# Performance work log

Measured on AMD Instinct MI355X. Metric: run time of the kernel, lower is better.

## Reference

```python
import jax, jax.numpy as jnp
import numpy as np

NUM_ITEMS = 50000
EMBED = 256
HEADS = 8
HEAD_DIM = EMBED // HEADS
B, S = 32, 512
NEG_BIG = -1e9   # mask fill for dot-product scores
NEG_SMALL = -1e5 # mask fill for rel / time maps (as in RKT)


def setup_inputs() -> dict:
    key = jax.random.key(0)
    ks = jax.random.split(key, 20)
    sc = 0.02
    return {
        "item_inputs": jax.random.randint(ks[0], (B, S), 0, NUM_ITEMS + 1),
        "label_inputs": jax.random.randint(ks[1], (B, S), 0, 2, dtype=jnp.int32),
        "item_ids": jax.random.randint(ks[2], (B, S), 0, NUM_ITEMS + 1),
        "rel": jax.random.uniform(ks[3], (B, S, S), jnp.float32),
        "timestamp": jax.random.uniform(ks[4], (B, S, S), jnp.float32) * 10.0,
        # learned params
        "item_embeds": jax.random.normal(ks[5], (NUM_ITEMS + 1, EMBED), jnp.float32) * sc,
        "W_in": jax.random.normal(ks[6], (2 * EMBED, EMBED), jnp.float32) * sc,
        "b_in": jnp.zeros((EMBED,), jnp.float32),
        "Wq": jax.random.normal(ks[7], (EMBED, EMBED), jnp.float32) * sc,
        "bq": jnp.zeros((EMBED,), jnp.float32),
        "Wk": jax.random.normal(ks[8], (EMBED, EMBED), jnp.float32) * sc,
        "bk": jnp.zeros((EMBED,), jnp.float32),
        "Wv": jax.random.normal(ks[9], (EMBED, EMBED), jnp.float32) * sc,
        "bv": jnp.zeros((EMBED,), jnp.float32),
        "W_out": jax.random.normal(ks[10], (EMBED, 1), jnp.float32) * sc,
        "b_out": jnp.zeros((1,), jnp.float32),
        "l1": jnp.float32(0.5),
        "l2": jnp.float32(0.5),
    }


def _split_heads(t, W, b):
    # [B,S,E] -> [B,H,S,HD]
    return (t @ W + b).reshape(B, S, HEADS, HEAD_DIM).transpose(0, 2, 1, 3)


def reference(item_inputs, label_inputs, item_ids, rel, timestamp, item_embeds,
              W_in, b_in, Wq, bq, Wk, bk, Wv, bv, W_out, b_out, l1, l2):
    # --- input construction: response-gated duplicated item embedding ---
    e = item_embeds[item_inputs]                       # [B,S,E]
    lab = label_inputs[..., None].astype(e.dtype)      # [B,S,1]
    inputs = jnp.concatenate([e * lab, e * (1.0 - lab)], axis=-1)  # [B,S,2E]
    inputs = jax.nn.relu(inputs @ W_in + b_in)         # [B,S,E]
    query = item_embeds[item_ids]                      # [B,S,E]

    future = jnp.triu(jnp.ones((S, S), bool), 1)       # True above diagonal

    Q = _split_heads(query, Wq, bq)
    K = _split_heads(inputs, Wk, bk)
    V = _split_heads(inputs, Wv, bv)

    # scaled dot-product scores with causal mask
    scores = jnp.einsum('bhqd,bhkd->bhqk', Q, K) / np.float32(np.sqrt(HEAD_DIM))
    prob_attn = jax.nn.softmax(jnp.where(future, NEG_BIG, scores), axis=-1)

    # relational (item-item correlation) attention, future-masked
    rel_m = rel * (~future).astype(rel.dtype)          # [B,S,S]
    rel_attn = jax.nn.softmax(jnp.where(rel_m == 0, NEG_SMALL, rel_m), axis=-1)
    rel_attn = rel_attn[:, None]                       # broadcast over heads

    # exponential time-decay attention, future-masked
    ts = jnp.exp(-jnp.abs(timestamp))
    time_attn = jax.nn.softmax(jnp.where(future, NEG_SMALL, ts), axis=-1)[:, None]

    attn = (1.0 - l2) * prob_attn + l2 * time_attn
    attn = (1.0 - l1) * attn + l1 * rel_attn           # [B,H,S,S]

    out = jnp.einsum('bhqk,bhkd->bhqd', attn, V)       # [B,H,S,HD]
    out = out.transpose(0, 2, 1, 3).reshape(B, S, EMBED)
    logits = out @ W_out + b_out                       # [B,S,1]
    return logits, attn
```

## Files before the change

kernel.cpp:

```cpp
#include <hip/hip_runtime.h>
#include <hip/hip_bf16.h>

#define SEQ 512
#define EMB 256
#define NHEAD 8
#define HD 32

using bf16x8 = __attribute__((ext_vector_type(8))) short;
using f32x4  = __attribute__((ext_vector_type(4))) float;

static __device__ __forceinline__ unsigned short f2bf(float x) {
    union { float f; unsigned int u; } v; v.f = x;
    unsigned int r = v.u + 0x7FFFu + ((v.u >> 16) & 1u);
    return (unsigned short)(r >> 16);
}
static __device__ __forceinline__ float bf2f(unsigned short v) {
    union { unsigned int u; float f; } w; w.u = ((unsigned int)v) << 16; return w.f;
}

__global__ __launch_bounds__(256) void fused_prep_kernel(
    const int* __restrict__ item_inputs,
    const int* __restrict__ label_inputs,
    const int* __restrict__ item_ids,
    const float* __restrict__ embeds,
    const float* __restrict__ W_in,
    const float* __restrict__ Wq,
    const float* __restrict__ Wk,
    const float* __restrict__ Wv,
    const float* __restrict__ Wout,
    const float* __restrict__ bv,
    const float* __restrict__ bout,
    const float* __restrict__ rel,
    const float* __restrict__ tsp,
    unsigned short* __restrict__ Abig,
    unsigned short* __restrict__ qbf,
    unsigned short* __restrict__ WTin,
    unsigned short* __restrict__ WTq,
    unsigned short* __restrict__ WTk,
    float* __restrict__ Wvw,
    float* __restrict__ bvw,
    float* __restrict__ logits,
    float* __restrict__ dent,
    float* __restrict__ denr)
{
    const int bid = blockIdx.x;
    const int t = threadIdx.x;

    if (bid < 1024) {
        const int b = bid >> 5;
        const int s16 = 31 - (bid & 31);
        const int q0 = s16 * 16;
        const int row = t >> 4;
        const int lane16 = t & 15;
        const int qrow = q0 + row;
        const size_t base = ((size_t)(b * SEQ) + qrow) * SEQ;
        float dt = 0.f, dr = 0.f;
        for (int k4 = lane16 * 4; k4 <= qrow; k4 += 64) {
            float4 tv4 = *(const float4*)(tsp + base + k4);
            float4 rv4 = *(const float4*)(rel + base + k4);
            const float* tvp = &tv4.x;
            const float* rvp = &rv4.x;
            #pragma unroll
            for (int j = 0; j < 4; j++) {
                const bool va = (k4 + j) <= qrow;
                dt += va ? __expf(__expf(-fabsf(tvp[j]))) : 0.f;
                dr += (va && rvp[j] != 0.f) ? __expf(rvp[j]) : 0.f;
            }
        }
        dt += __shfl_xor(dt, 1); dt += __shfl_xor(dt, 2);
        dt += __shfl_xor(dt, 4); dt += __shfl_xor(dt, 8);
        dr += __shfl_xor(dr, 1); dr += __shfl_xor(dr, 2);
        dr += __shfl_xor(dr, 4); dr += __shfl_xor(dr, 8);
        if (lane16 == 0) {
            dent[b * SEQ + qrow] = dt;
            denr[b * SEQ + qrow] = dr;
        }
    } else if (bid < 5120) {
        int r = (bid - 1024) * 4 + (t >> 6);
        int j = (t & 63) * 4;
        int item = item_inputs[r];
        int lab  = label_inputs[r];
        int qid  = item_ids[r];
        float4 e4 = *(const float4*)(embeds + (size_t)item * EMB + j);
        ushort4 on  = make_ushort4(f2bf(e4.x), f2bf(e4.y), f2bf(e4.z), f2bf(e4.w));
        ushort4 off = make_ushort4(0, 0, 0, 0);
        *(ushort4*)(Abig + (size_t)r * 512 + j)       = lab ? on : off;
        *(ushort4*)(Abig + (size_t)r * 512 + 256 + j) = lab ? off : on;
        float4 q4 = *(const float4*)(embeds + (size_t)qid * EMB + j);
        *(ushort4*)(qbf + (size_t)r * 256 + j) =
            make_ushort4(f2bf(q4.x), f2bf(q4.y), f2bf(q4.z), f2bf(q4.w));
    } else {
        int idx = (bid - 5120) * 256 + t;
        if (idx < 131072) {
            int n = idx >> 9, k = idx & 511;
            WTin[idx] = f2bf(W_in[(size_t)k * 256 + n]);
        } else if (idx < 196608) {
            int i = idx - 131072;
            int n = i >> 8, k = i & 255;
            WTq[i] = f2bf(Wq[(size_t)k * 256 + n]);
        } else if (idx < 262144) {
            int i = idx - 196608;
            int n = i >> 8, k = i & 255;
            WTk[i] = f2bf(Wk[(size_t)k * 256 + n]);
        } else if (idx < 264192) {
            int i = idx - 262144;
            int c = i >> 3, h = i & 7;
            float s = 0.f;
            #pragma unroll
            for (int d = 0; d < 32; d++)
                s += Wv[(size_t)c * 256 + h * 32 + d] * Wout[h * 32 + d];
            Wvw[i] = s;
        } else if (idx < 264200) {
            int h = idx - 264192;
            float s = 0.f;
            #pragma unroll
            for (int d = 0; d < 32; d++) s += bv[h * 32 + d] * Wout[h * 32 + d];
            bvw[h] = s;
        } else if (idx < 280584) {
            logits[idx - 264200] = bout[0];
        }
    }
}

template<int KDIM, int RELU, int OUTBF>
static __device__ __forceinline__ void gemm_body(
    const unsigned short* __restrict__ A,
    const unsigned short* __restrict__ BT,
    const float* __restrict__ bias,
    void* __restrict__ Cout, float scale)
{
    __shared__ unsigned short As[64][40];
    __shared__ unsigned short Bs[128][40];
    const int t = threadIdx.x;
    const int row0 = blockIdx.x * 64;
    const int col0 = blockIdx.y * 128;
    const int wid = t >> 6, lane = t & 63;
    const int wm = wid & 1, wn = wid >> 1;
    const int lg = lane >> 4, l15 = lane & 15;

    f32x4 acc[2][4];
    #pragma unroll
    for (int i = 0; i < 2; i++)
        #pragma unroll
        for (int j = 0; j < 4; j++) acc[i][j] = (f32x4){0.f, 0.f, 0.f, 0.f};

    const int arow = t >> 2, achk = t & 3;
    const int brow = t >> 1, bhalf = t & 1;

    for (int k0 = 0; k0 < KDIM; k0 += 32) {
        __syncthreads();
        *(uint4*)(&As[arow][achk * 8]) =
            *(const uint4*)(A + (size_t)(row0 + arow) * KDIM + k0 + achk * 8);
        const unsigned short* bsrc = BT + (size_t)(col0 + brow) * KDIM + k0 + bhalf * 16;
        *(uint4*)(&Bs[brow][bhalf * 16])     = *(const uint4*)(bsrc);
        *(uint4*)(&Bs[brow][bhalf * 16 + 8]) = *(const uint4*)(bsrc + 8);
        __syncthreads();
        bf16x8 af[2], bfr[4];
        #pragma unroll
        for (int fm = 0; fm < 2; fm++)
            af[fm] = *(const bf16x8*)(&As[wm * 32 + fm * 16 + l15][lg * 8]);
        #pragma unroll
        for (int fn = 0; fn < 4; fn++)
            bfr[fn] = *(const bf16x8*)(&Bs[wn * 64 + fn * 16 + l15][lg * 8]);
        #pragma unroll
        for (int fm = 0; fm < 2; fm++)
            #pragma unroll
            for (int fn = 0; fn < 4; fn++)
                acc[fm][fn] = __builtin_amdgcn_mfma_f32_16x16x32_bf16(
                    af[fm], bfr[fn], acc[fm][fn], 0, 0, 0);
    }
    #pragma unroll
    for (int fm = 0; fm < 2; fm++)
        #pragma unroll
        for (int fn = 0; fn < 4; fn++) {
            int col = col0 + wn * 64 + fn * 16 + l15;
            float bvv = bias[col];
            #pragma unroll
            for (int r = 0; r < 4; r++) {
                int row = row0 + wm * 32 + fm * 16 + lg * 4 + r;
                float v = acc[fm][fn][r] + bvv;
                if (RELU) v = fmaxf(v, 0.f);
                v *= scale;
                if (OUTBF) ((unsigned short*)Cout)[(size_t)row * 256 + col] = f2bf(v);
                else       ((float*)Cout)[(size_t)row * 256 + col] = v;
            }
        }
}

__global__ __launch_bounds__(256, 2) void gemmA_kernel(
    const unsigned short* __restrict__ Abig,
    const unsigned short* __restrict__ WTin,
    const float* __restrict__ b_in,
    unsigned short* __restrict__ Xbf,
    const unsigned short* __restrict__ qbf,
    const unsigned short* __restrict__ WTq,
    const float* __restrict__ bq,
    unsigned short* __restrict__ Qbf)
{
    if (blockIdx.z == 0)
        gemm_body<512, 1, 1>(Abig, WTin, b_in, (void*)Xbf, 1.0f);
    else
        gemm_body<256, 0, 1>(qbf, WTq, bq, (void*)Qbf, 0.17677669529663687f);
}

static __device__ __forceinline__ void vw_body(
    const unsigned short* __restrict__ Xbf,
    const float* __restrict__ Wvw,
    const float* __restrict__ bvw,
    float* __restrict__ Vw)
{
    __shared__ float sW[2048];
    __shared__ float sb[8];
    int t = threadIdx.x;
    #pragma unroll
    for (int i = 0; i < 8; i++) sW[i * 256 + t] = Wvw[i * 256 + t];
    if (t < 8) sb[t] = bvw[t];
    __syncthreads();
    int row = blockIdx.x * 256 + t;
    float acc[8];
    #pragma unroll
    for (int h = 0; h < 8; h++) acc[h] = sb[h];
    for (int d0 = 0; d0 < 32; d0++) {
        bf16x8 x = *(const bf16x8*)(Xbf + (size_t)row * 256 + d0 * 8);
        #pragma unroll
        for (int j = 0; j < 8; j++) {
            float xf = bf2f((unsigned short)x[j]);
            #pragma unroll
            for (int h = 0; h < 8; h++) acc[h] += xf * sW[(d0 * 8 + j) * 8 + h];
        }
    }
    *(float4*)(Vw + (size_t)row * 8)     = make_float4(acc[0], acc[1], acc[2], acc[3]);
    *(float4*)(Vw + (size_t)row * 8 + 4) = make_float4(acc[4], acc[5], acc[6], acc[7]);
}

__global__ __launch_bounds__(256, 2) void gemmB_kernel(
    const unsigned short* __restrict__ Xbf,
    const unsigned short* __restrict__ WTk,
    const float* __restrict__ bk,
    unsigned short* __restrict__ Kbf,
    const float* __restrict__ Wvw,
    const float* __restrict__ bvw,
    float* __restrict__ Vw)
{
    if (blockIdx.z == 0) {
        gemm_body<256, 0, 1>(Xbf, WTk, bk, (void*)Kbf, 1.0f);
    } else {
        if (blockIdx.x >= 64 || blockIdx.y != 0) return;
        vw_body(Xbf, Wvw, bvw, Vw);
    }
}

__global__ __launch_bounds__(256, 8) void attnW_kernel(
    const unsigned short* __restrict__ Qbf,
    const unsigned short* __restrict__ Kbf,
    const float* __restrict__ Vw,
    const float* __restrict__ rel,
    const float* __restrict__ tsp,
    const float* __restrict__ dent,
    const float* __restrict__ denr,
    const float* __restrict__ pl1,
    const float* __restrict__ pl2,
    float* __restrict__ logits,
    float* __restrict__ attn)
{
    __shared__ unsigned short sP[16][520];
    __shared__ float sVw[512];
    __shared__ float sden[4][16];

    const int t = threadIdx.x;
    const int id = blockIdx.x;
    const int qt16 = 31 - (id >> 8);
    const int b = (id >> 3) & 31;
    const int h = id & 7;
    const int q0 = qt16 * 16;
    const int qmax = q0 + 15;

    const int w = t >> 6, lane = t & 63;
    const int l15 = lane & 15, lg = lane >> 4;

    const float l1 = pl1[0], l2 = pl2[0];
    const float cp = (1.f - l1) * (1.f - l2);
    const float ct = (1.f - l1) * l2;
    const float cr = l1;

    sVw[t]       = Vw[((size_t)(b * SEQ) + t) * 8 + h];
    sVw[256 + t] = Vw[((size_t)(b * SEQ) + 256 + t) * 8 + h];

    bf16x8 aq = *(const bf16x8*)(Qbf + (size_t)(b * SEQ + q0 + l15) * EMB + h * 32 + lg * 8);

    float dp[4] = {0.f, 0.f, 0.f, 0.f};
    #pragma unroll
    for (int ki = 0; ki < 4; ki++) {
        const int kt = w + ki * 4;
        const int k0 = kt * 32;
        if (k0 <= qmax) {
            #pragma unroll
            for (int nf = 0; nf < 2; nf++) {
                const int kcol = k0 + nf * 16 + l15;
                bf16x8 bk = *(const bf16x8*)(Kbf +
                    (size_t)(b * SEQ + kcol) * EMB + h * 32 + lg * 8);
                f32x4 am = __builtin_amdgcn_mfma_f32_16x16x32_bf16(
                    aq, bk, (f32x4){0.f, 0.f, 0.f, 0.f}, 0, 0, 0);
                #pragma unroll
                for (int r = 0; r < 4; r++) {
                    const int qloc = lg * 4 + r;
                    float e = (kcol <= q0 + qloc) ? __expf(am[r]) : 0.f;
                    sP[qloc][kcol] = f2bf(e);
                    dp[r] += e;
                }
            }
        } else {
            #pragma unroll
            for (int nf = 0; nf < 2; nf++)
                #pragma unroll
                for (int r = 0; r < 4; r++)
                    sP[lg * 4 + r][k0 + nf * 16 + l15] = 0;
        }
    }
    #pragma unroll
    for (int r = 0; r < 4; r++) {
        float v = dp[r];
        v += __shfl_xor(v, 1); v += __shfl_xor(v, 2);
        v += __shfl_xor(v, 4); v += __shfl_xor(v, 8);
        if (l15 == 0) sden[w][lg * 4 + r] = v;
    }
    __syncthreads();

    const int wrow = t >> 4;
    const int wcol = (t & 15) * 4;
    const int qrow_w = q0 + wrow;
    const float den = sden[0][wrow] + sden[1][wrow] + sden[2][wrow] + sden[3][wrow];
    const float cpinv = cp / den;
    const float dtv = dent[b * SEQ + qrow_w];
    const float drv = denr[b * SEQ + qrow_w];
    const float ctt = ct / dtv;
    const float crr = drv > 0.f ? cr / drv : 0.f;

    float* arow = attn + ((size_t)((b * NHEAD + h) * SEQ) + qrow_w) * SEQ;
    const size_t rbase = ((size_t)(b * SEQ) + qrow_w) * SEQ;
    const f32x4 z4 = (f32x4){0.f, 0.f, 0.f, 0.f};
    float plog = 0.f;

    #pragma unroll
    for (int s = 0; s < 8; s++) {
        const int c = wcol + s * 64;
        f32x4 o;
        if (c > qrow_w) {
            o = z4;
        } else {
            float4 tv4 = *(const float4*)(tsp + rbase + c);
            float4 rv4 = *(const float4*)(rel + rbase + c);
            ushort4 p4 = *(const ushort4*)(&sP[wrow][c]);
            const float* tvp = &tv4.x;
            const float* rvp = &rv4.x;
            const unsigned short* pp = &p4.x;
            #pragma unroll
            for (int j = 0; j < 4; j++) {
                const bool va = (c + j) <= qrow_w;
                float e_t = va ? __expf(__expf(-fabsf(tvp[j]))) * ctt : 0.f;
                float e_r = (va && rvp[j] != 0.f) ? __expf(rvp[j]) * crr : 0.f;
                float a = fmaf(bf2f(pp[j]), cpinv, e_t + e_r);
                a = va ? a : 0.f;
                o[j] = a;
                plog = fmaf(a, sVw[c + j], plog);
            }
        }
        __builtin_nontemporal_store(o, (f32x4*)(arow + c));
    }

    plog += __shfl_xor(plog, 1); plog += __shfl_xor(plog, 2);
    plog += __shfl_xor(plog, 4); plog += __shfl_xor(plog, 8);
    if ((t & 15) == 0)
        atomicAdd(&logits[b * SEQ + qrow_w], plog);
}

extern "C" void kernel_launch(void* const* d_in, const int* in_sizes, int n_in,
                              void* d_out, int out_size, void* d_ws, size_t ws_size,
                              hipStream_t stream)
{
    (void)in_sizes; (void)n_in; (void)out_size; (void)ws_size;
    const int*   item_inputs  = (const int*)d_in[0];
    const int*   label_inputs = (const int*)d_in[1];
    const int*   item_ids     = (const int*)d_in[2];
    const float* rel   = (const float*)d_in[3];
    const float* tsp   = (const float*)d_in[4];
    const float* emb   = (const float*)d_in[5];
    const float* W_in  = (const float*)d_in[6];
    const float* b_in  = (const float*)d_in[7];
    const float* Wq    = (const float*)d_in[8];
    const float* bq    = (const float*)d_in[9];
    const float* Wk    = (const float*)d_in[10];
    const float* bk    = (const float*)d_in[11];
    const float* Wv    = (const float*)d_in[12];
    const float* bv    = (const float*)d_in[13];
    const float* Wout  = (const float*)d_in[14];
    const float* bout  = (const float*)d_in[15];
    const float* l1    = (const float*)d_in[16];
    const float* l2    = (const float*)d_in[17];

    const size_t R = 16384;
    char* w = (char*)d_ws;
    unsigned short* Abig = (unsigned short*)w; w += R * 512 * 2;
    unsigned short* qbf  = (unsigned short*)w; w += R * 256 * 2;
    unsigned short* WTin = (unsigned short*)w; w += (size_t)256 * 512 * 2;
    unsigned short* WTq  = (unsigned short*)w; w += (size_t)256 * 256 * 2;
    unsigned short* WTk  = (unsigned short*)w; w += (size_t)256 * 256 * 2;
    unsigned short* Xbf  = (unsigned short*)w; w += R * 256 * 2;
    unsigned short* Qbf  = (unsigned short*)w; w += R * 256 * 2;
    unsigned short* Kbf  = (unsigned short*)w; w += R * 256 * 2;
    float* Wvw  = (float*)w; w += 2048 * 4;
    float* Vw   = (float*)w; w += R * 8 * 4;
    float* bvw  = (float*)w; w += 256;
    float* dent = (float*)w; w += (size_t)32 * SEQ * 4;
    float* denr = (float*)w; w += (size_t)32 * SEQ * 4;

    float* logits = (float*)d_out;
    float* attnp  = (float*)d_out + 16384;

    fused_prep_kernel<<<dim3(6217), dim3(256), 0, stream>>>(
        item_inputs, label_inputs, item_ids, emb,
        W_in, Wq, Wk, Wv, Wout, bv, bout, rel, tsp,
        Abig, qbf, WTin, WTq, WTk, Wvw, bvw, logits, dent, denr);

    gemmA_kernel<<<dim3(256, 2, 2), dim3(256), 0, stream>>>(
        Abig, WTin, b_in, Xbf, qbf, WTq, bq, Qbf);

    gemmB_kernel<<<dim3(256, 2, 2), dim3(256), 0, stream>>>(
        Xbf, WTk, bk, Kbf, Wvw, bvw, Vw);

    attnW_kernel<<<dim3(8192), dim3(256), 0, stream>>>(
        Qbf, Kbf, Vw, rel, tsp, dent, denr, l1, l2, logits, attnp);
}
```

Baseline: 145.2 us.

## Offload zero-fill of upper-triangular attention tiles into earlier kernels

The strictly-future 64x64 tiles of the attention output are now zero-filled with nontemporal stores by extra blocks added to the prep and the two GEMM kernels. The attention kernel then loops only up to the diagonal tile for each row and skips zeroing the softmax scratch beyond it. The goal is to take the zero-write bandwidth off the critical attention kernel and overlap it with compute-light stages. This adds cross-kernel coupling through tile-index bookkeeping, and the grids must stay exactly in step with that bookkeeping.

After: 227.1 us. +56.4%, slower.

```diff
diff --git a/kernel.cpp b/kernel.cpp
--- a/kernel.cpp
+++ b/kernel.cpp
@@ -16,6 +16,34 @@
 }
 static __device__ __forceinline__ float bf2f(unsigned short v) {
     union { unsigned int u; float f; } w; w.u = ((unsigned int)v) << 16; return w.f;
+}
+
+static __device__ __forceinline__ void zfill_work(int idx, int t,
+                                                  float* __restrict__ attn)
+{
+    const f32x4 z4 = (f32x4){0.f, 0.f, 0.f, 0.f};
+    #pragma unroll
+    for (int i = 0; i < 4; i++) {
+        int ti = idx * 4 + i;
+        int bh = ti / 28;
+        int tt = ti - bh * 28;
+        int s = 0, pre = 0;
+        #pragma unroll
+        for (int ss = 0; ss < 6; ss++) {
+            int cnt = 7 - s;
+            bool adv = tt >= pre + cnt;
+            pre += adv ? cnt : 0;
+            s   += adv ? 1 : 0;
+        }
+        int j = tt - pre;
+        int row = 64 * s + (t >> 2);
+        int col = 64 * (s + 1) + 64 * j + (t & 3) * 16;
+        float* p = attn + ((size_t)bh * SEQ + row) * SEQ + col;
+        __builtin_nontemporal_store(z4, (f32x4*)(p));
+        __builtin_nontemporal_store(z4, (f32x4*)(p + 4));
+        __builtin_nontemporal_store(z4, (f32x4*)(p + 8));
+        __builtin_nontemporal_store(z4, (f32x4*)(p + 12));
+    }
 }
 
 __global__ __launch_bounds__(256) void fused_prep_kernel(
@@ -41,7 +69,8 @@
     float* __restrict__ bvw,
     float* __restrict__ logits,
     float* __restrict__ dent,
-    float* __restrict__ denr)
+    float* __restrict__ denr,
+    float* __restrict__ attn)
 {
     const int bid = blockIdx.x;
     const int t = threadIdx.x;
@@ -89,7 +118,7 @@
         float4 q4 = *(const float4*)(embeds + (size_t)qid * EMB + j);
         *(ushort4*)(qbf + (size_t)r * 256 + j) =
             make_ushort4(f2bf(q4.x), f2bf(q4.y), f2bf(q4.z), f2bf(q4.w));
-    } else {
+    } else if (bid < 6217) {
         int idx = (bid - 5120) * 256 + t;
         if (idx < 131072) {
             int n = idx >> 9, k = idx & 511;
@@ -119,6 +148,8 @@
         } else if (idx < 280584) {
             logits[idx - 264200] = bout[0];
         }
+    } else {
+        zfill_work(bid - 6217, t, attn);
     }
 }
 
@@ -195,12 +226,15 @@
     const unsigned short* __restrict__ qbf,
     const unsigned short* __restrict__ WTq,
     const float* __restrict__ bq,
-    unsigned short* __restrict__ Qbf)
+    unsigned short* __restrict__ Qbf,
+    float* __restrict__ attn)
 {
     if (blockIdx.z == 0)
         gemm_body<512, 1, 1>(Abig, WTin, b_in, (void*)Xbf, 1.0f);
+    else if (blockIdx.z == 1)
+        gemm_body<256, 0, 1>(qbf, WTq, bq, (void*)Qbf, 0.17677669529663687f);
     else
-        gemm_body<256, 0, 1>(qbf, WTq, bq, (void*)Qbf, 0.17677669529663687f);
+        zfill_work(768 + (blockIdx.y << 8) + blockIdx.x, threadIdx.x, attn);
 }
 
 static __device__ __forceinline__ void vw_body(
@@ -240,13 +274,16 @@
     unsigned short* __restrict__ Kbf,
     const float* __restrict__ Wvw,
     const float* __restrict__ bvw,
-    float* __restrict__ Vw)
+    float* __restrict__ Vw,
+    float* __restrict__ attn)
 {
     if (blockIdx.z == 0) {
         gemm_body<256, 0, 1>(Xbf, WTk, bk, (void*)Kbf, 1.0f);
-    } else {
+    } else if (blockIdx.z == 1) {
         if (blockIdx.x >= 64 || blockIdx.y != 0) return;
         vw_body(Xbf, Wvw, bvw, Vw);
+    } else {
+        zfill_work(1280 + (blockIdx.y << 8) + blockIdx.x, threadIdx.x, attn);
     }
 }
 
@@ -309,7 +346,7 @@
                     dp[r] += e;
                 }
             }
-        } else {
+        } else if (k0 <= qmax + 64) {
             #pragma unroll
             for (int nf = 0; nf < 2; nf++)
                 #pragma unroll
@@ -329,6 +366,7 @@
     const int wrow = t >> 4;
     const int wcol = (t & 15) * 4;
     const int qrow_w = q0 + wrow;
+    const int smax = qrow_w >> 6;
     const float den = sden[0][wrow] + sden[1][wrow] + sden[2][wrow] + sden[3][wrow];
     const float cpinv = cp / den;
     const float dtv = dent[b * SEQ + qrow_w];
@@ -341,8 +379,7 @@
     const f32x4 z4 = (f32x4){0.f, 0.f, 0.f, 0.f};
     float plog = 0.f;
 
-    #pragma unroll
-    for (int s = 0; s < 8; s++) {
+    for (int s = 0; s <= smax; s++) {
         const int c = wcol + s * 64;
         f32x4 o;
         if (c > qrow_w) {
@@ -417,16 +454,16 @@
     float* logits = (float*)d_out;
     float* attnp  = (float*)d_out + 16384;
 
-    fused_prep_kernel<<<dim3(6217), dim3(256), 0, stream>>>(
+    fused_prep_kernel<<<dim3(6985), dim3(256), 0, stream>>>(
         item_inputs, label_inputs, item_ids, emb,
         W_in, Wq, Wk, Wv, Wout, bv, bout, rel, tsp,
-        Abig, qbf, WTin, WTq, WTk, Wvw, bvw, logits, dent, denr);
-
-    gemmA_kernel<<<dim3(256, 2, 2), dim3(256), 0, stream>>>(
-        Abig, WTin, b_in, Xbf, qbf, WTq, bq, Qbf);
-
-    gemmB_kernel<<<dim3(256, 2, 2), dim3(256), 0, stream>>>(
-        Xbf, WTk, bk, Kbf, Wvw, bvw, Vw);
+        Abig, qbf, WTin, WTq, WTk, Wvw, bvw, logits, dent, denr, attnp);
+
+    gemmA_kernel<<<dim3(256, 2, 3), dim3(256), 0, stream>>>(
+        Abig, WTin, b_in, Xbf, qbf, WTq, bq, Qbf, attnp);
+
+    gemmB_kernel<<<dim3(256, 2, 3), dim3(256), 0, stream>>>(
+        Xbf, WTk, bk, Kbf, Wvw, bvw, Vw, attnp);
 
     attnW_kernel<<<dim3(8192), dim3(256), 0, stream>>>(
         Qbf, Kbf, Vw, rel, tsp, dent, denr, l1, l2, logits, attnp);
```

## Fuse head loop into attention kernel and cache rel/time numerators in LDS

Applied to the files above, without the earlier changes.

The time/rel softmax denominator pass moves out of the prep kernel and into the attention kernel. Each block now handles one (batch, 16-query tile) and loops over all 8 heads, so the rel and timestamp rows are read from global memory once instead of once per head. Their exponentials are stored as packed bf16 in shared memory, and Vw is written head-major so it can be loaded directly. Logits are written directly instead of accumulated atomically. The trade-offs are fewer blocks (1024) with larger LDS use and lower occupancy, a serial head loop with two barriers per head, and bf16 rounding of the rel/time numerators.

Result: slower. 150.2 us (+3.4%).

```diff
diff --git a/kernel.cpp b/kernel.cpp
--- a/kernel.cpp
+++ b/kernel.cpp
@@ -30,8 +30,6 @@
     const float* __restrict__ Wout,
     const float* __restrict__ bv,
     const float* __restrict__ bout,
-    const float* __restrict__ rel,
-    const float* __restrict__ tsp,
     unsigned short* __restrict__ Abig,
     unsigned short* __restrict__ qbf,
     unsigned short* __restrict__ WTin,
@@ -39,44 +37,13 @@
     unsigned short* __restrict__ WTk,
     float* __restrict__ Wvw,
     float* __restrict__ bvw,
-    float* __restrict__ logits,
-    float* __restrict__ dent,
-    float* __restrict__ denr)
+    float* __restrict__ logits)
 {
     const int bid = blockIdx.x;
     const int t = threadIdx.x;
 
-    if (bid < 1024) {
-        const int b = bid >> 5;
-        const int s16 = 31 - (bid & 31);
-        const int q0 = s16 * 16;
-        const int row = t >> 4;
-        const int lane16 = t & 15;
-        const int qrow = q0 + row;
-        const size_t base = ((size_t)(b * SEQ) + qrow) * SEQ;
-        float dt = 0.f, dr = 0.f;
-        for (int k4 = lane16 * 4; k4 <= qrow; k4 += 64) {
-            float4 tv4 = *(const float4*)(tsp + base + k4);
-            float4 rv4 = *(const float4*)(rel + base + k4);
-            const float* tvp = &tv4.x;
-            const float* rvp = &rv4.x;
-            #pragma unroll
-            for (int j = 0; j < 4; j++) {
-                const bool va = (k4 + j) <= qrow;
-                dt += va ? __expf(__expf(-fabsf(tvp[j]))) : 0.f;
-                dr += (va && rvp[j] != 0.f) ? __expf(rvp[j]) : 0.f;
-            }
-        }
-        dt += __shfl_xor(dt, 1); dt += __shfl_xor(dt, 2);
-        dt += __shfl_xor(dt, 4); dt += __shfl_xor(dt, 8);
-        dr += __shfl_xor(dr, 1); dr += __shfl_xor(dr, 2);
-        dr += __shfl_xor(dr, 4); dr += __shfl_xor(dr, 8);
-        if (lane16 == 0) {
-            dent[b * SEQ + qrow] = dt;
-            denr[b * SEQ + qrow] = dr;
-        }
-    } else if (bid < 5120) {
-        int r = (bid - 1024) * 4 + (t >> 6);
+    if (bid < 4096) {
+        int r = bid * 4 + (t >> 6);
         int j = (t & 63) * 4;
         int item = item_inputs[r];
         int lab  = label_inputs[r];
@@ -90,7 +57,7 @@
         *(ushort4*)(qbf + (size_t)r * 256 + j) =
             make_ushort4(f2bf(q4.x), f2bf(q4.y), f2bf(q4.z), f2bf(q4.w));
     } else {
-        int idx = (bid - 5120) * 256 + t;
+        int idx = (bid - 4096) * 256 + t;
         if (idx < 131072) {
             int n = idx >> 9, k = idx & 511;
             WTin[idx] = f2bf(W_in[(size_t)k * 256 + n]);
@@ -207,7 +174,7 @@
     const unsigned short* __restrict__ Xbf,
     const float* __restrict__ Wvw,
     const float* __restrict__ bvw,
-    float* __restrict__ Vw)
+    float* __restrict__ VwT)
 {
     __shared__ float sW[2048];
     __shared__ float sb[8];
@@ -229,8 +196,10 @@
             for (int h = 0; h < 8; h++) acc[h] += xf * sW[(d0 * 8 + j) * 8 + h];
         }
     }
-    *(float4*)(Vw + (size_t)row * 8)     = make_float4(acc[0], acc[1], acc[2], acc[3]);
-    *(float4*)(Vw + (size_t)row * 8 + 4) = make_float4(acc[4], acc[5], acc[6], acc[7]);
+    const int bb = row >> 9, rr = row & 511;
+    #pragma unroll
+    for (int h = 0; h < 8; h++)
+        VwT[((size_t)(bb * NHEAD + h)) * SEQ + rr] = acc[h];
 }
 
 __global__ __launch_bounds__(256, 2) void gemmB_kernel(
@@ -240,38 +209,37 @@
     unsigned short* __restrict__ Kbf,
     const float* __restrict__ Wvw,
     const float* __restrict__ bvw,
-    float* __restrict__ Vw)
+    float* __restrict__ VwT)
 {
     if (blockIdx.z == 0) {
         gemm_body<256, 0, 1>(Xbf, WTk, bk, (void*)Kbf, 1.0f);
     } else {
         if (blockIdx.x >= 64 || blockIdx.y != 0) return;
-        vw_body(Xbf, Wvw, bvw, Vw);
-    }
-}
-
-__global__ __launch_bounds__(256, 8) void attnW_kernel(
+        vw_body(Xbf, Wvw, bvw, VwT);
+    }
+}
+
+__global__ __launch_bounds__(256, 3) void attnF_kernel(
     const unsigned short* __restrict__ Qbf,
     const unsigned short* __restrict__ Kbf,
-    const float* __restrict__ Vw,
+    const float* __restrict__ VwT,
     const float* __restrict__ rel,
     const float* __restrict__ tsp,
-    const float* __restrict__ dent,
-    const float* __restrict__ denr,
+    const float* __restrict__ bout,
     const float* __restrict__ pl1,
     const float* __restrict__ pl2,
     float* __restrict__ logits,
     float* __restrict__ attn)
 {
+    __shared__ unsigned int   sNum[16][520];
     __shared__ unsigned short sP[16][520];
-    __shared__ float sVw[512];
     __shared__ float sden[4][16];
+    __shared__ float sctt[16], scrr[16];
 
     const int t = threadIdx.x;
     const int id = blockIdx.x;
-    const int qt16 = 31 - (id >> 8);
-    const int b = (id >> 3) & 31;
-    const int h = id & 7;
+    const int b = id >> 5;
+    const int qt16 = 31 - (id & 31);
     const int q0 = qt16 * 16;
     const int qmax = q0 + 15;
 
@@ -283,95 +251,115 @@
     const float ct = (1.f - l1) * l2;
     const float cr = l1;
 
-    sVw[t]       = Vw[((size_t)(b * SEQ) + t) * 8 + h];
-    sVw[256 + t] = Vw[((size_t)(b * SEQ) + 256 + t) * 8 + h];
-
-    bf16x8 aq = *(const bf16x8*)(Qbf + (size_t)(b * SEQ + q0 + l15) * EMB + h * 32 + lg * 8);
-
-    float dp[4] = {0.f, 0.f, 0.f, 0.f};
-    #pragma unroll
-    for (int ki = 0; ki < 4; ki++) {
-        const int kt = w + ki * 4;
-        const int k0 = kt * 32;
-        if (k0 <= qmax) {
-            #pragma unroll
-            for (int nf = 0; nf < 2; nf++) {
-                const int kcol = k0 + nf * 16 + l15;
-                bf16x8 bk = *(const bf16x8*)(Kbf +
-                    (size_t)(b * SEQ + kcol) * EMB + h * 32 + lg * 8);
-                f32x4 am = __builtin_amdgcn_mfma_f32_16x16x32_bf16(
-                    aq, bk, (f32x4){0.f, 0.f, 0.f, 0.f}, 0, 0, 0);
+    const int wrow = t >> 4;
+    const int lane16 = t & 15;
+    const int qrow_w = q0 + wrow;
+    const size_t rbase = ((size_t)(b * SEQ) + qrow_w) * SEQ;
+
+    float dt = 0.f, dr = 0.f;
+    for (int k4 = lane16 * 4; k4 <= qrow_w; k4 += 64) {
+        float4 tv4 = *(const float4*)(tsp + rbase + k4);
+        float4 rv4 = *(const float4*)(rel + rbase + k4);
+        const float* tvp = &tv4.x;
+        const float* rvp = &rv4.x;
+        unsigned int pk[4];
+        #pragma unroll
+        for (int j = 0; j < 4; j++) {
+            const bool va = (k4 + j) <= qrow_w;
+            float et = va ? __expf(__expf(-fabsf(tvp[j]))) : 0.f;
+            float er = (va && rvp[j] != 0.f) ? __expf(rvp[j]) : 0.f;
+            dt += et; dr += er;
+            pk[j] = (unsigned int)f2bf(et) | ((unsigned int)f2bf(er) << 16);
+        }
+        *(uint4*)(&sNum[wrow][k4]) = make_uint4(pk[0], pk[1], pk[2], pk[3]);
+    }
+    dt += __shfl_xor(dt, 1); dt += __shfl_xor(dt, 2);
+    dt += __shfl_xor(dt, 4); dt += __shfl_xor(dt, 8);
+    dr += __shfl_xor(dr, 1); dr += __shfl_xor(dr, 2);
+    dr += __shfl_xor(dr, 4); dr += __shfl_xor(dr, 8);
+    if (lane16 == 0) {
+        sctt[wrow] = ct / dt;
+        scrr[wrow] = dr > 0.f ? cr / dr : 0.f;
+    }
+
+    const f32x4 z4 = (f32x4){0.f, 0.f, 0.f, 0.f};
+    float plog = 0.f;
+
+    #pragma unroll 1
+    for (int h = 0; h < 8; h++) {
+        bf16x8 aq = *(const bf16x8*)(Qbf +
+            (size_t)(b * SEQ + q0 + l15) * EMB + h * 32 + lg * 8);
+        float dp[4] = {0.f, 0.f, 0.f, 0.f};
+        #pragma unroll
+        for (int ki = 0; ki < 4; ki++) {
+            const int k0 = (w + ki * 4) * 32;
+            if (k0 <= qmax) {
                 #pragma unroll
-                for (int r = 0; r < 4; r++) {
-                    const int qloc = lg * 4 + r;
-                    float e = (kcol <= q0 + qloc) ? __expf(am[r]) : 0.f;
-                    sP[qloc][kcol] = f2bf(e);
-                    dp[r] += e;
+                for (int nf = 0; nf < 2; nf++) {
+                    const int kcol = k0 + nf * 16 + l15;
+                    bf16x8 bk = *(const bf16x8*)(Kbf +
+                        (size_t)(b * SEQ + kcol) * EMB + h * 32 + lg * 8);
+                    f32x4 am = __builtin_amdgcn_mfma_f32_16x16x32_bf16(
+                        aq, bk, (f32x4){0.f, 0.f, 0.f, 0.f}, 0, 0, 0);
+                    #pragma unroll
+                    for (int r = 0; r < 4; r++) {
+                        const int qloc = lg * 4 + r;
+                        float e = (kcol <= q0 + qloc) ? __expf(am[r]) : 0.f;
+                        sP[qloc][kcol] = f2bf(e);
+                        dp[r] += e;
+                    }
                 }
             }
-        } else {
-            #pragma unroll
-            for (int nf = 0; nf < 2; nf++)
+        }
+        #pragma unroll
+        for (int r = 0; r < 4; r++) {
+            float v = dp[r];
+            v += __shfl_xor(v, 1); v += __shfl_xor(v, 2);
+            v += __shfl_xor(v, 4); v += __shfl_xor(v, 8);
+            if (l15 == 0) sden[w][lg * 4 + r] = v;
+        }
+        __syncthreads();
+
+        const float den = sden[0][wrow] + sden[1][wrow] + sden[2][wrow] + sden[3][wrow];
+        const float cpinv = cp / den;
+        const float ctt = sctt[wrow];
+        const float crr = scrr[wrow];
+        float* arow = attn + ((size_t)((b * NHEAD + h) * SEQ) + qrow_w) * SEQ;
+        const float* vwh = VwT + ((size_t)(b * NHEAD + h)) * SEQ;
+
+        #pragma unroll
+        for (int s = 0; s < 8; s++) {
+            const int c = lane16 * 4 + s * 64;
+            f32x4 o;
+            if (c > qrow_w) {
+                o = z4;
+            } else {
+                uint4   nv = *(const uint4*)(&sNum[wrow][c]);
+                ushort4 p4 = *(const ushort4*)(&sP[wrow][c]);
+                float4  v4 = *(const float4*)(vwh + c);
+                const unsigned int* np = &nv.x;
+                const unsigned short* pp = &p4.x;
+                const float* vp = &v4.x;
                 #pragma unroll
-                for (int r = 0; r < 4; r++)
-                    sP[lg * 4 + r][k0 + nf * 16 + l15] = 0;
-        }
-    }
-    #pragma unroll
-    for (int r = 0; r < 4; r++) {
-        float v = dp[r];
-        v += __shfl_xor(v, 1); v += __shfl_xor(v, 2);
-        v += __shfl_xor(v, 4); v += __shfl_xor(v, 8);
-        if (l15 == 0) sden[w][lg * 4 + r] = v;
-    }
-    __syncthreads();
-
-    const int wrow = t >> 4;
-    const int wcol = (t & 15) * 4;
-    const int qrow_w = q0 + wrow;
-    const float den = sden[0][wrow] + sden[1][wrow] + sden[2][wrow] + sden[3][wrow];
-    const float cpinv = cp / den;
-    const float dtv = dent[b * SEQ + qrow_w];
-    const float drv = denr[b * SEQ + qrow_w];
-    const float ctt = ct / dtv;
-    const float crr = drv > 0.f ? cr / drv : 0.f;
-
-    float* arow = attn + ((size_t)((b * NHEAD + h) * SEQ) + qrow_w) * SEQ;
-    const size_t rbase = ((size_t)(b * SEQ) + qrow_w) * SEQ;
-    const f32x4 z4 = (f32x4){0.f, 0.f, 0.f, 0.f};
-    float plog = 0.f;
-
-    #pragma unroll
-    for (int s = 0; s < 8; s++) {
-        const int c = wcol + s * 64;
-        f32x4 o;
-        if (c > qrow_w) {
-            o = z4;
-        } else {
-            float4 tv4 = *(const float4*)(tsp + rbase + c);
-            float4 rv4 = *(const float4*)(rel + rbase + c);
-            ushort4 p4 = *(const ushort4*)(&sP[wrow][c]);
-            const float* tvp = &tv4.x;
-            const float* rvp = &rv4.x;
-            const unsigned short* pp = &p4.x;
-            #pragma unroll
-            for (int j = 0; j < 4; j++) {
-                const bool va = (c + j) <= qrow_w;
-                float e_t = va ? __expf(__expf(-fabsf(tvp[j]))) * ctt : 0.f;
-                float e_r = (va && rvp[j] != 0.f) ? __expf(rvp[j]) * crr : 0.f;
-                float a = fmaf(bf2f(pp[j]), cpinv, e_t + e_r);
-                a = va ? a : 0.f;
-                o[j] = a;
-                plog = fmaf(a, sVw[c + j], plog);
+                for (int j = 0; j < 4; j++) {
+                    const bool va = (c + j) <= qrow_w;
+                    float et = bf2f((unsigned short)(np[j] & 0xffffu));
+                    float er = bf2f((unsigned short)(np[j] >> 16));
+                    float a = fmaf(bf2f(pp[j]), cpinv, fmaf(et, ctt, er * crr));
+                    a = va ? a : 0.f;
+                    o[j] = a;
+                    plog = fmaf(a, vp[j], plog);
+                }
             }
-        }
-        __builtin_nontemporal_store(o, (f32x4*)(arow + c));
+            __builtin_nontemporal_store(o, (f32x4*)(arow + c));
+        }
+        __syncthreads();
     }
 
     plog += __shfl_xor(plog, 1); plog += __shfl_xor(plog, 2);
     plog += __shfl_xor(plog, 4); plog += __shfl_xor(plog, 8);
-    if ((t & 15) == 0)
-        atomicAdd(&logits[b * SEQ + qrow_w], plog);
+    if (lane16 == 0)
+        logits[b * SEQ + qrow_w] = bout[0] + plog;
 }
 
 extern "C" void kernel_launch(void* const* d_in, const int* in_sizes, int n_in,
@@ -409,25 +397,23 @@
     unsigned short* Qbf  = (unsigned short*)w; w += R * 256 * 2;
     unsigned short* Kbf  = (unsigned short*)w; w += R * 256 * 2;
     float* Wvw  = (float*)w; w += 2048 * 4;
-    float* Vw   = (float*)w; w += R * 8 * 4;
+    float* VwT  = (float*)w; w += R * 8 * 4;
     float* bvw  = (float*)w; w += 256;
-    float* dent = (float*)w; w += (size_t)32 * SEQ * 4;
-    float* denr = (float*)w; w += (size_t)32 * SEQ * 4;
 
     float* logits = (float*)d_out;
     float* attnp  = (float*)d_out + 16384;
 
-    fused_prep_kernel<<<dim3(6217), dim3(256), 0, stream>>>(
+    fused_prep_kernel<<<dim3(5193), dim3(256), 0, stream>>>(
         item_inputs, label_inputs, item_ids, emb,
-        W_in, Wq, Wk, Wv, Wout, bv, bout, rel, tsp,
-        Abig, qbf, WTin, WTq, WTk, Wvw, bvw, logits, dent, denr);
+        W_in, Wq, Wk, Wv, Wout, bv, bout,
+        Abig, qbf, WTin, WTq, WTk, Wvw, bvw, logits);
 
     gemmA_kernel<<<dim3(256, 2, 2), dim3(256), 0, stream>>>(
         Abig, WTin, b_in, Xbf, qbf, WTq, bq, Qbf);
 
     gemmB_kernel<<<dim3(256, 2, 2), dim3(256), 0, stream>>>(
-        Xbf, WTk, bk, Kbf, Wvw, bvw, Vw);
-
-    attnW_kernel<<<dim3(8192), dim3(256), 0, stream>>>(
-        Qbf, Kbf, Vw, rel, tsp, dent, denr, l1, l2, logits, attnp);
-}
+        Xbf, WTk, bk, Kbf, Wvw, bvw, VwT);
+
+    attnF_kernel<<<dim3(1024), dim3(256), 0, stream>>>(
+        Qbf, Kbf, VwT, rel, tsp, bout, l1, l2, logits, attnp);
+}
```
